# Optimization experiments

Measured on AMD Instinct MI355X. Metric: run time of the kernel, lower is better.

Reference implementation:

```python
import jax, jax.numpy as jnp
import numpy as np

MODEL_BATCHES = 2048
NUM_POINTS = 8192
N_FUNCS = 8
REMOVE_ITERS = 51  # remove_points = 51 * model_batches -> first 51 iterations dropped


def setup_inputs() -> dict:
    key = jax.random.key(0)
    k1, k2, k3, k4, k5 = jax.random.split(key, 5)
    point = jax.random.normal(k1, (MODEL_BATCHES, 2, 1), dtype=jnp.float32) * 0.1
    optimized_weights = jax.random.normal(k2, (N_FUNCS, 2, 2), dtype=jnp.float32) * 0.5
    optimized_biases = jax.random.normal(k3, (N_FUNCS, 2, 1), dtype=jnp.float32) * 0.5
    optimized_function_ops = jax.random.uniform(k4, (N_FUNCS,), dtype=jnp.float32)
    index = jax.random.randint(k5, (MODEL_BATCHES, NUM_POINTS), 0, N_FUNCS, dtype=jnp.int32)
    return {
        "point": point,
        "optimized_weights": optimized_weights,
        "optimized_biases": optimized_biases,
        "optimized_function_ops": optimized_function_ops,
        "index": index,
    }


def reference(point, optimized_weights, optimized_biases, optimized_function_ops, index):
    mb = point.shape[0]

    def step(p, idx):  # p: [mb,2,1], idx: [mb]
        W = optimized_weights[idx]          # [mb,2,2]
        b = optimized_biases[idx]           # [mb,2,1]
        op = optimized_function_ops[idx]    # [mb]
        p_new = jnp.einsum('bij,bjk->bik', W, p) + b  # [mb,2,1]
        out = jnp.concatenate([p_new[:, :, 0], op[:, None]], axis=1)  # [mb,3]
        return p_new, out

    # scan over iterations: index.T is [num_points, mb]
    _, outs = jax.lax.scan(step, point, index.T)  # outs: [num_points, mb, 3]
    pts = outs.reshape(-1, 3)  # matches torch.cat along dim 0 then squeeze
    return pts[REMOVE_ITERS * mb:, :]
```

## Files before the change

### kernel.cpp

```cpp
#include <hip/hip_runtime.h>

#define MB   2048
#define NP   8192
#define NF   8
#define RM   51
#define NCH  128
#define CH   64
#define COLS 17

typedef float          f32x4 __attribute__((ext_vector_type(4)));
typedef unsigned int   u32;
typedef unsigned short u16;

#define CMAP(g) ((((g) & 7) << 1) | ((g) >> 3))


__device__ __forceinline__ void build_tbl(float4* tA, float4* tB, const float* W,
                                          const float* B, const float* OPS, int tid)
{
    if (tid < NF) {
        tA[tid] = make_float4(W[tid*4+0], W[tid*4+1], W[tid*4+2], W[tid*4+3]);
        tB[tid] = make_float4(B[tid*2+0], B[tid*2+1], OPS ? OPS[tid] : 0.f, 0.f);
    }
}

__device__ __forceinline__ void stage_u16(
    const int* __restrict__ idxg, u16 (*tile)[COLS],
    int c, int b0, int x8, int yy, int seg)
{
    #pragma unroll
    for (int p = 0; p < 8; ++p) {
        const int row = yy + p * 32;
        const int4 v = *(const int4*)(idxg + (size_t)(b0 + row) * NP
                                      + c * CH + seg * 32 + x8 * 4);
        tile[row][2 * x8 + seg] = (u16)(v.x | (v.y << 4) | (v.z << 8) | (v.w << 12));
    }
}

__global__ __launch_bounds__(256, 4) void ifs_phase1(
    const int* __restrict__ idxg, const float* __restrict__ W,
    const float* __restrict__ B,
    float4* __restrict__ mapsA, float2* __restrict__ mapsC)
{
    __shared__ u16 tile[256][COLS];
    __shared__ __align__(16) float4 tA[NF], tB[NF];
    const int tid = threadIdx.x;
    const int c   = blockIdx.x >> 3;
    const int b0  = (blockIdx.x & 7) << 8;
    const int x8  = tid & 7, yy = tid >> 3;

    build_tbl(tA, tB, W, B, nullptr, tid);
    stage_u16(idxg, tile, c, b0, x8, yy, 0);
    __syncthreads();

    float a00 = 1.f, a01 = 0.f, a10 = 0.f, a11 = 1.f, c0 = 0.f, c1 = 0.f;
    for (int seg = 0; seg < 2; ++seg) {
        if (seg == 0) stage_u16(idxg, tile, c, b0, x8, yy, 1);
        #pragma unroll
        for (int j = 0; j < 8; ++j) {
            const u32 pc = tile[tid][CMAP(seg * 8 + j)];
            #pragma unroll
            for (int e = 0; e < 4; ++e) {
                const int f = (pc >> (4 * e)) & 7;
                const float4 w  = tA[f];
                const float4 bb = tB[f];
                const float na00 = w.x*a00 + w.y*a10;
                const float na01 = w.x*a01 + w.y*a11;
                const float na10 = w.z*a00 + w.w*a10;
                const float na11 = w.z*a01 + w.w*a11;
                const float nc0  = w.x*c0  + w.y*c1 + bb.x;
                const float nc1  = w.z*c0  + w.w*c1 + bb.y;
                a00 = na00; a01 = na01; a10 = na10; a11 = na11; c0 = nc0; c1 = nc1;
            }
        }
        __syncthreads();
    }
    mapsA[(size_t)c * MB + b0 + tid] = make_float4(a00, a01, a10, a11);
    mapsC[(size_t)c * MB + b0 + tid] = make_float2(c0, c1);
}

__global__ __launch_bounds__(64) void ifs_phase2(
    const float2* __restrict__ point, const float4* __restrict__ mapsA,
    const float2* __restrict__ mapsC, float2* __restrict__ pe)
{
    const int b = blockIdx.x * 64 + threadIdx.x;
    float2 p = point[b];
    float4 A0[8], A1[8]; float2 C0[8], C1[8];
    #pragma unroll
    for (int k = 0; k < 8; ++k) {
        A0[k] = mapsA[(size_t)k * MB + b];
        C0[k] = mapsC[(size_t)k * MB + b];
    }
    for (int g = 0; g < 16; ++g) {
        if (g < 15) {
            #pragma unroll
            for (int k = 0; k < 8; ++k) {
                A1[k] = mapsA[(size_t)((g + 1) * 8 + k) * MB + b];
                C1[k] = mapsC[(size_t)((g + 1) * 8 + k) * MB + b];
            }
        }
        #pragma unroll
        for (int k = 0; k < 8; ++k) {
            pe[(size_t)(g * 8 + k) * MB + b] = p;
            const float nx = A0[k].x * p.x + A0[k].y * p.y + C0[k].x;
            const float ny = A0[k].z * p.x + A0[k].w * p.y + C0[k].y;
            p.x = nx; p.y = ny;
        }
        #pragma unroll
        for (int k = 0; k < 8; ++k) { A0[k] = A1[k]; C0[k] = C1[k]; }
    }
}

__global__ __launch_bounds__(256, 4) void ifs_phase3(
    const int* __restrict__ idxg, const float* __restrict__ W,
    const float* __restrict__ B, const float* __restrict__ OPS,
    const float2* __restrict__ pe, float* __restrict__ out)
{
    __shared__ u16 tile[256][COLS];
    __shared__ __align__(16) float sbuf[2][4][256][3];
    __shared__ __align__(16) float4 tA[NF], tB[NF];
    const int tid = threadIdx.x;
    const int c   = blockIdx.x >> 3;
    const int b0  = (blockIdx.x & 7) << 8;
    const int x8  = tid & 7, yy = tid >> 3;

    build_tbl(tA, tB, W, B, OPS, tid);
    stage_u16(idxg, tile, c, b0, x8, yy, 0);
    stage_u16(idxg, tile, c, b0, x8, yy, 1);

    float2 p = pe[(size_t)c * MB + b0 + tid];

    int s_[3];
    long long off[3];
    #pragma unroll
    for (int k = 0; k < 3; ++k) {
        const int w = 4 * (tid + 256 * k);
        s_[k] = w / 768;
        const int r = w - s_[k] * 768;
        off[k] = (long long)(c * CH + s_[k] - RM) * (MB * 3) + b0 * 3 + r;
    }
    const bool chk = (c == 0);
    __syncthreads();

    for (int g = 0; g < 16; ++g) {
        const int buf = g & 1;
        const u32 pc = tile[tid][CMAP(g)];
        #pragma unroll
        for (int s = 0; s < 4; ++s) {
            const int f = (pc >> (4 * s)) & 7;
            const float4 w  = tA[f];
            const float4 bb = tB[f];
            const float nx = w.x * p.x + w.y * p.y + bb.x;
            const float ny = w.z * p.x + w.w * p.y + bb.y;
            p.x = nx; p.y = ny;
            sbuf[buf][s][tid][0] = nx;
            sbuf[buf][s][tid][1] = ny;
            sbuf[buf][s][tid][2] = bb.z;
        }
        __syncthreads();
        const float* flat = &sbuf[buf][0][0][0];
        #pragma unroll
        for (int k = 0; k < 3; ++k) {
            if (!chk || (g * 4 + s_[k]) >= RM) {
                const f32x4 v = *(const f32x4*)(flat + 4 * (tid + 256 * k));
                __builtin_nontemporal_store(v, (f32x4*)(out + off[k]));
            }
            off[k] += 4LL * (MB * 3);
        }
    }
}

extern "C" void kernel_launch(void* const* d_in, const int* in_sizes, int n_in,
                              void* d_out, int out_size, void* d_ws, size_t ws_size,
                              hipStream_t stream) {
    const float2* point = (const float2*)d_in[0];
    const float*  W     = (const float*)d_in[1];
    const float*  B     = (const float*)d_in[2];
    const float*  OPS   = (const float*)d_in[3];
    const int*    idx   = (const int*)  d_in[4];
    float*        out   = (float*)d_out;

    char* ws = (char*)d_ws;
    float4* mapsA = (float4*)(ws);
    float2* mapsC = (float2*)(ws + (size_t)NCH * MB * 16);
    float2* pe    = (float2*)(ws + (size_t)NCH * MB * 24);

    ifs_phase1<<<NCH * (MB / 256), 256, 0, stream>>>(idx, W, B, mapsA, mapsC);
    ifs_phase2<<<MB / 64, 64, 0, stream>>>(point, mapsA, mapsC, pe);
    ifs_phase3<<<NCH * (MB / 256), 256, 0, stream>>>(idx, W, B, OPS, pe, out);
}
```

Measured before the change: 86.05 us.

## Merge prefix scan into replay kernel and cache packed index codes

Restructures the three-phase chunked affine scan into two kernels. The compose kernel now uses 128-step chunks, and it also writes the packed 4-bit index codes to workspace. The replay kernel has each block compute its own chunk start point by applying all earlier chunk maps serially, instead of relying on a separate single-wave prefix kernel. This removes one launch, the narrow serial phase-2 kernel, and the second full read of the int32 index array. In exchange, late chunks do redundant prefix work of up to 63 map applications, and occupancy hints are lowered.

New measurement: 71.49 us. 1.2x faster.

```diff
diff --git a/kernel.cpp b/kernel.cpp
--- a/kernel.cpp
+++ b/kernel.cpp
@@ -4,15 +4,15 @@
 #define NP   8192
 #define NF   8
 #define RM   51
-#define NCH  128
-#define CH   64
-#define COLS 17
+#define NCH  64
+#define CH   128
+#define COLS 33
 
 typedef float          f32x4 __attribute__((ext_vector_type(4)));
 typedef unsigned int   u32;
 typedef unsigned short u16;
 
-#define CMAP(g) ((((g) & 7) << 1) | ((g) >> 3))
+#define CMAP(g) ((((g) & 7) << 2) | ((g) >> 3))
 
 
 __device__ __forceinline__ void build_tbl(float4* tA, float4* tB, const float* W,
@@ -33,20 +33,21 @@
         const int row = yy + p * 32;
         const int4 v = *(const int4*)(idxg + (size_t)(b0 + row) * NP
                                       + c * CH + seg * 32 + x8 * 4);
-        tile[row][2 * x8 + seg] = (u16)(v.x | (v.y << 4) | (v.z << 8) | (v.w << 12));
+        tile[row][4 * x8 + seg] = (u16)(v.x | (v.y << 4) | (v.z << 8) | (v.w << 12));
     }
 }
 
-__global__ __launch_bounds__(256, 4) void ifs_phase1(
+__global__ __launch_bounds__(256, 2) void ifs_compose(
     const int* __restrict__ idxg, const float* __restrict__ W,
     const float* __restrict__ B,
-    float4* __restrict__ mapsA, float2* __restrict__ mapsC)
+    float4* __restrict__ mapsA, float2* __restrict__ mapsC, u32* __restrict__ codes)
 {
     __shared__ u16 tile[256][COLS];
     __shared__ __align__(16) float4 tA[NF], tB[NF];
     const int tid = threadIdx.x;
     const int c   = blockIdx.x >> 3;
     const int b0  = (blockIdx.x & 7) << 8;
+    const int b   = b0 + tid;
     const int x8  = tid & 7, yy = tid >> 3;
 
     build_tbl(tA, tB, W, B, nullptr, tid);
@@ -54,8 +55,8 @@
     __syncthreads();
 
     float a00 = 1.f, a01 = 0.f, a10 = 0.f, a11 = 1.f, c0 = 0.f, c1 = 0.f;
-    for (int seg = 0; seg < 2; ++seg) {
-        if (seg == 0) stage_u16(idxg, tile, c, b0, x8, yy, 1);
+    for (int seg = 0; seg < 4; ++seg) {
+        if (seg < 3) stage_u16(idxg, tile, c, b0, x8, yy, seg + 1);
         #pragma unroll
         for (int j = 0; j < 8; ++j) {
             const u32 pc = tile[tid][CMAP(seg * 8 + j)];
@@ -75,60 +76,62 @@
         }
         __syncthreads();
     }
-    mapsA[(size_t)c * MB + b0 + tid] = make_float4(a00, a01, a10, a11);
-    mapsC[(size_t)c * MB + b0 + tid] = make_float2(c0, c1);
+    #pragma unroll
+    for (int j = 0; j < 16; ++j) {
+        const u32 w = (u32)tile[tid][CMAP(2 * j)]
+                    | ((u32)tile[tid][CMAP(2 * j + 1)] << 16);
+        codes[((size_t)c * 16 + j) * MB + b] = w;
+    }
+    mapsA[(size_t)c * MB + b] = make_float4(a00, a01, a10, a11);
+    mapsC[(size_t)c * MB + b] = make_float2(c0, c1);
 }
 
-__global__ __launch_bounds__(64) void ifs_phase2(
+__global__ __launch_bounds__(256, 2) void ifs_replay(
     const float2* __restrict__ point, const float4* __restrict__ mapsA,
-    const float2* __restrict__ mapsC, float2* __restrict__ pe)
+    const float2* __restrict__ mapsC, const u32* __restrict__ codes,
+    const float* __restrict__ W, const float* __restrict__ B,
+    const float* __restrict__ OPS, float* __restrict__ out)
 {
-    const int b = blockIdx.x * 64 + threadIdx.x;
-    float2 p = point[b];
-    float4 A0[8], A1[8]; float2 C0[8], C1[8];
-    #pragma unroll
-    for (int k = 0; k < 8; ++k) {
-        A0[k] = mapsA[(size_t)k * MB + b];
-        C0[k] = mapsC[(size_t)k * MB + b];
-    }
-    for (int g = 0; g < 16; ++g) {
-        if (g < 15) {
-            #pragma unroll
-            for (int k = 0; k < 8; ++k) {
-                A1[k] = mapsA[(size_t)((g + 1) * 8 + k) * MB + b];
-                C1[k] = mapsC[(size_t)((g + 1) * 8 + k) * MB + b];
-            }
-        }
-        #pragma unroll
-        for (int k = 0; k < 8; ++k) {
-            pe[(size_t)(g * 8 + k) * MB + b] = p;
-            const float nx = A0[k].x * p.x + A0[k].y * p.y + C0[k].x;
-            const float ny = A0[k].z * p.x + A0[k].w * p.y + C0[k].y;
-            p.x = nx; p.y = ny;
-        }
-        #pragma unroll
-        for (int k = 0; k < 8; ++k) { A0[k] = A1[k]; C0[k] = C1[k]; }
-    }
-}
-
-__global__ __launch_bounds__(256, 4) void ifs_phase3(
-    const int* __restrict__ idxg, const float* __restrict__ W,
-    const float* __restrict__ B, const float* __restrict__ OPS,
-    const float2* __restrict__ pe, float* __restrict__ out)
-{
-    __shared__ u16 tile[256][COLS];
     __shared__ __align__(16) float sbuf[2][4][256][3];
     __shared__ __align__(16) float4 tA[NF], tB[NF];
     const int tid = threadIdx.x;
     const int c   = blockIdx.x >> 3;
     const int b0  = (blockIdx.x & 7) << 8;
-    const int x8  = tid & 7, yy = tid >> 3;
+    const int b   = b0 + tid;
 
     build_tbl(tA, tB, W, B, OPS, tid);
-    stage_u16(idxg, tile, c, b0, x8, yy, 0);
-    stage_u16(idxg, tile, c, b0, x8, yy, 1);
 
-    float2 p = pe[(size_t)c * MB + b0 + tid];
+    u32 cw[16];
+    #pragma unroll
+    for (int j = 0; j < 16; ++j)
+        cw[j] = codes[((size_t)c * 16 + j) * MB + b];
+
+    float2 p = point[b];
+    {
+        int k = 0;
+        float4 Ab[8]; float2 Cb[8];
+        while (k + 8 <= c) {
+            #pragma unroll
+            for (int j = 0; j < 8; ++j) {
+                Ab[j] = mapsA[(size_t)(k + j) * MB + b];
+                Cb[j] = mapsC[(size_t)(k + j) * MB + b];
+            }
+            #pragma unroll
+            for (int j = 0; j < 8; ++j) {
+                const float nx = Ab[j].x * p.x + Ab[j].y * p.y + Cb[j].x;
+                const float ny = Ab[j].z * p.x + Ab[j].w * p.y + Cb[j].y;
+                p.x = nx; p.y = ny;
+            }
+            k += 8;
+        }
+        for (; k < c; ++k) {
+            const float4 A = mapsA[(size_t)k * MB + b];
+            const float2 C = mapsC[(size_t)k * MB + b];
+            const float nx = A.x * p.x + A.y * p.y + C.x;
+            const float ny = A.z * p.x + A.w * p.y + C.y;
+            p.x = nx; p.y = ny;
+        }
+    }
 
     int s_[3];
     long long off[3];
@@ -142,9 +145,9 @@
     const bool chk = (c == 0);
     __syncthreads();
 
-    for (int g = 0; g < 16; ++g) {
+    for (int g = 0; g < 32; ++g) {
         const int buf = g & 1;
-        const u32 pc = tile[tid][CMAP(g)];
+        const u32 pc = cw[g >> 1] >> ((g & 1) * 16);
         #pragma unroll
         for (int s = 0; s < 4; ++s) {
             const int f = (pc >> (4 * s)) & 7;
@@ -183,9 +186,9 @@
     char* ws = (char*)d_ws;
     float4* mapsA = (float4*)(ws);
     float2* mapsC = (float2*)(ws + (size_t)NCH * MB * 16);
-    float2* pe    = (float2*)(ws + (size_t)NCH * MB * 24);
+    u32*    codes = (u32*)   (ws + (size_t)NCH * MB * 24);
 
-    ifs_phase1<<<NCH * (MB / 256), 256, 0, stream>>>(idx, W, B, mapsA, mapsC);
-    ifs_phase2<<<MB / 64, 64, 0, stream>>>(point, mapsA, mapsC, pe);
-    ifs_phase3<<<NCH * (MB / 256), 256, 0, stream>>>(idx, W, B, OPS, pe, out);
+    ifs_compose<<<NCH * (MB / 256), 256, 0, stream>>>(idx, W, B, mapsA, mapsC, codes);
+    ifs_replay <<<NCH * (MB / 256), 256, 0, stream>>>(point, mapsA, mapsC, codes,
+                                                      W, B, OPS, out);
 }
```
